# Performance work log

Hardware: AMD Instinct MI355X
Metric: run time of the kernel (lower is better)

## Reference

```python
import jax, jax.numpy as jnp
import numpy as np

DIM = 384
HEADS = 6
HEAD_DIM = DIM // HEADS
HIDDEN = 4 * DIM
K_NEIGH = 8
EPS = 1e-5


def layer_norm(x, w, b):
    mu = jnp.mean(x, axis=-1, keepdims=True)
    var = jnp.mean(jnp.square(x - mu), axis=-1, keepdims=True)
    return (x - mu) * jax.lax.rsqrt(var + EPS) * w + b


def setup_inputs() -> dict:
    key = jax.random.key(0)
    ks = jax.random.split(key, 16)
    B, N, D = 8, 2048, DIM
    s = 0.02
    inp = {
        "x": jax.random.normal(ks[0], (B, N, D), dtype=jnp.float32),
        "knn_index": jax.random.randint(ks[1], (B * K_NEIGH * N,), 0, B * N, dtype=jnp.int64),
        "norm1_w": jnp.ones((D,), jnp.float32),
        "norm1_b": jnp.zeros((D,), jnp.float32),
        "qkv_w": jax.random.normal(ks[2], (D, 3 * D), jnp.float32) * s,
        "proj_w": jax.random.normal(ks[3], (D, D), jnp.float32) * s,
        "proj_b": jnp.zeros((D,), jnp.float32),
        "knn_w": jax.random.normal(ks[4], (2 * D, D), jnp.float32) * s,
        "knn_b": jnp.zeros((D,), jnp.float32),
        "merge_w": jax.random.normal(ks[5], (2 * D, D), jnp.float32) * s,
        "merge_b": jnp.zeros((D,), jnp.float32),
        "norm2_w": jnp.ones((D,), jnp.float32),
        "norm2_b": jnp.zeros((D,), jnp.float32),
        "fc1_w": jax.random.normal(ks[6], (D, HIDDEN), jnp.float32) * s,
        "fc1_b": jnp.zeros((HIDDEN,), jnp.float32),
        "fc2_w": jax.random.normal(ks[7], (HIDDEN, D), jnp.float32) * s,
        "fc2_b": jnp.zeros((D,), jnp.float32),
    }
    return inp


def _forward(x, knn_index, norm1_w, norm1_b, qkv_w, proj_w, proj_b,
             knn_w, knn_b, merge_w, merge_b, norm2_w, norm2_b,
             fc1_w, fc1_b, fc2_w, fc2_b):
    B, N, D = x.shape
    norm_x = layer_norm(x, norm1_w, norm1_b)

    # --- multi-head self-attention (no qkv bias, no dropout) ---
    qkv = (norm_x @ qkv_w).reshape(B, N, 3, HEADS, HEAD_DIM)
    q, k, v = qkv[:, :, 0], qkv[:, :, 1], qkv[:, :, 2]  # [B,N,H,Dh]
    scale = HEAD_DIM ** -0.5
    attn = jnp.einsum("bnhd,bmhd->bhnm", q, k) * scale
    attn = jax.nn.softmax(attn, axis=-1)
    x_1 = jnp.einsum("bhnm,bmhd->bnhd", attn, v).reshape(B, N, D)
    x_1 = x_1 @ proj_w + proj_b

    # --- graph feature: gather k=8 neighbors, diff-concat ---
    feat = norm_x.reshape(B * N, D)[knn_index].reshape(B, K_NEIGH, N, D)
    xq = norm_x[:, None]  # [B,1,N,D]
    knn_f = jnp.concatenate([feat - xq, jnp.broadcast_to(xq, feat.shape)], axis=-1)
    knn_f = jax.nn.leaky_relu(knn_f @ knn_w + knn_b, negative_slope=0.2)
    knn_f = jnp.max(knn_f, axis=1)  # max-pool over neighbors -> [B,N,D]

    x_1 = jnp.concatenate([x_1, knn_f], axis=-1) @ merge_w + merge_b
    x = x + x_1

    # --- MLP block ---
    h = layer_norm(x, norm2_w, norm2_b)
    h = jax.nn.gelu(h @ fc1_w + fc1_b, approximate=False)
    x = x + (h @ fc2_w + fc2_b)
    return x


def reference(x, knn_index, norm1_w, norm1_b, qkv_w, proj_w, proj_b,
              knn_w, knn_b, merge_w, merge_b, norm2_w, norm2_b,
              fc1_w, fc1_b, fc2_w, fc2_b):
    return _forward(x, knn_index, norm1_w, norm1_b, qkv_w, proj_w, proj_b,
                    knn_w, knn_b, merge_w, merge_b, norm2_w, norm2_b,
                    fc1_w, fc1_b, fc2_w, fc2_b)
```

## Files before the change

kernel.cpp:

```cpp
#include <hip/hip_runtime.h>

typedef unsigned short u16;
typedef unsigned int u32;
typedef __attribute__((ext_vector_type(8))) short short8;
typedef __attribute__((ext_vector_type(4))) u16 u16x4;
typedef __attribute__((ext_vector_type(2))) u32 u32x2;
typedef __attribute__((ext_vector_type(4))) float f32x4;

__device__ __forceinline__ u16 f2bf(float f) {
  unsigned u = __float_as_uint(f);
  u += 0x7fffu + ((u >> 16) & 1u);
  return (u16)(u >> 16);
}
__device__ __forceinline__ float b2f(u16 v) { return __uint_as_float((u32)v << 16); }

#define GLD16(g, l)                                                        \
  __builtin_amdgcn_global_load_lds(                                        \
      (const __attribute__((address_space(1))) void*)(g),                  \
      (__attribute__((address_space(3))) void*)(l), 16, 0, 0)

struct TJobs {
  const float* in[7];
  unsigned long long outoff[7];
  int ld[7], row0[7], K[7], blkend[7];
};
__global__ void transpose_all_kernel(TJobs J, char* __restrict__ ws) {
  int bx = blockIdx.x;
  int ji = 0;
  while (bx >= J.blkend[ji]) ji++;
  int base = (ji == 0) ? 0 : J.blkend[ji - 1];
  int i = (bx - base) * 256 + threadIdx.x;
  int K = J.K[ji];
  int j = i / K, k = i - j * K;
  u16* out = (u16*)(ws + J.outoff[ji]);
  out[(size_t)j * K + k] = f2bf(J.in[ji][(size_t)(J.row0[ji] + k) * J.ld[ji] + j]);
}

__global__ void ln_kernel(const float* __restrict__ in, const float* __restrict__ w,
                          const float* __restrict__ b, u16* __restrict__ out) {
  int row = blockIdx.x, t = threadIdx.x;
  const float* r = in + (size_t)row * 384;
  float v[6];
  float s = 0.f;
#pragma unroll
  for (int i = 0; i < 6; i++) { v[i] = r[t + 64 * i]; s += v[i]; }
#pragma unroll
  for (int off = 32; off > 0; off >>= 1) s += __shfl_xor(s, off);
  float mu = s * (1.f / 384.f);
  float q = 0.f;
#pragma unroll
  for (int i = 0; i < 6; i++) { float d = v[i] - mu; q += d * d; }
#pragma unroll
  for (int off = 32; off > 0; off >>= 1) q += __shfl_xor(q, off);
  float rstd = rsqrtf(q * (1.f / 384.f) + 1e-5f);
#pragma unroll
  for (int i = 0; i < 6; i++) {
    int j = t + 64 * i;
    out[(size_t)row * 384 + j] = f2bf((v[i] - mu) * rstd * w[j] + b[j]);
  }
}

template <int MODE, int TN>
__global__ __launch_bounds__(256) void gemm_kernel(
    const u16* __restrict__ A, const u16* __restrict__ Bt,
    int M, int N, int K, int ldc,
    const float* __restrict__ bias, const float* __restrict__ res,
    void* __restrict__ out0, void* __restrict__ out1, void* __restrict__ out2,
    void* __restrict__ out3) {
  __shared__ u16 Als[2][128 * 32];
  __shared__ u16 Bls[2][TN * 32];
  const int NJ = TN / 32;
  const int MB = M >> 7;
  int mb = blockIdx.x % MB, nb = blockIdx.x / MB;
  int m0 = mb << 7, n0 = nb * TN;
  int tid = threadIdx.x;
  int lane = tid & 63, w = tid >> 6;
  int wm = (w >> 1) << 6, wn = (w & 1) * (TN / 2);
  int l15 = lane & 15, l16 = lane >> 4;
  const f32x4 fz = {0.f, 0.f, 0.f, 0.f};
  f32x4 acc[4][NJ];
#pragma unroll
  for (int i = 0; i < 4; i++)
#pragma unroll
    for (int j = 0; j < NJ; j++) acc[i][j] = fz;

  const int strow = lane >> 2, stch = (lane & 3) * 8;
  const u16* Ag = A + (size_t)(m0 + w * 32 + strow) * K + stch;
  const u16* Bg = Bt + (size_t)(n0 + w * (TN / 4) + strow) * K + stch;
  u16* Al0 = &Als[0][(w * 32) * 32];
  u16* Al1 = &Als[1][(w * 32) * 32];
  u16* Bl0 = &Bls[0][(w * (TN / 4)) * 32];
  u16* Bl1 = &Bls[1][(w * (TN / 4)) * 32];

  for (int k0 = 0; k0 < K; k0 += 64) {
    __syncthreads();
    GLD16(Ag + k0, Al0);
    GLD16(Ag + k0 + (size_t)16 * K, Al0 + 16 * 32);
    GLD16(Ag + k0 + 32, Al1);
    GLD16(Ag + k0 + 32 + (size_t)16 * K, Al1 + 16 * 32);
    GLD16(Bg + k0, Bl0);
    GLD16(Bg + k0 + 32, Bl1);
    if (TN == 128) {
      GLD16(Bg + k0 + (size_t)16 * K, Bl0 + 16 * 32);
      GLD16(Bg + k0 + 32 + (size_t)16 * K, Bl1 + 16 * 32);
    }
    asm volatile("s_waitcnt vmcnt(0)" ::: "memory");
    __syncthreads();
#pragma unroll
    for (int kk = 0; kk < 2; kk++) {
      short8 af[4], bfr[NJ];
#pragma unroll
      for (int i = 0; i < 4; i++)
        af[i] = *(const short8*)&Als[kk][(wm + i * 16 + l15) * 32 + l16 * 8];
#pragma unroll
      for (int j = 0; j < NJ; j++)
        bfr[j] = *(const short8*)&Bls[kk][(wn + j * 16 + l15) * 32 + l16 * 8];
      __builtin_amdgcn_s_setprio(1);
#pragma unroll
      for (int i = 0; i < 4; i++)
#pragma unroll
        for (int j = 0; j < NJ; j++)
          acc[i][j] = __builtin_amdgcn_mfma_f32_16x16x32_bf16(af[i], bfr[j], acc[i][j], 0, 0, 0);
      __builtin_amdgcn_s_setprio(0);
    }
  }

#pragma unroll
  for (int i = 0; i < 4; i++)
#pragma unroll
    for (int j = 0; j < NJ; j++)
#pragma unroll
      for (int r = 0; r < 4; r++) {
        int row = m0 + wm + i * 16 + l16 * 4 + r;
        int col = n0 + wn + j * 16 + l15;
        float v = acc[i][j][r];
        if (MODE == 1) {
          ((u16*)out0)[(size_t)row * ldc + col] = f2bf(v + bias[col]);
        } else if (MODE == 2) {
          if (col < 384) {
            ((u16*)out0)[(size_t)row * 384 + col] = f2bf(v * 0.18033688011112042f);
          } else if (col < 768) {
            ((u16*)out1)[(size_t)row * 384 + col - 384] = f2bf(v);
          } else if (col < 1152) {
            int df = col - 768, hh = df >> 6, dd = df & 63;
            ((u16*)out2)[(((size_t)(row >> 11) * 6 + hh) * 64 + dd) * 2048 + (row & 2047)] = f2bf(v);
          } else {
            ((u16*)out3)[(size_t)row * 768 + (col - 1152)] = f2bf(v);
          }
        } else if (MODE == 3) {
          ((float*)out0)[(size_t)row * ldc + col] = v + bias[col] + res[(size_t)row * ldc + col];
        } else if (MODE == 4) {
          float u = v + bias[col];
          float t = u * (0.79788456f + 0.03567741f * u * u);
          float g = u / (1.f + exp2f(-2.88539008f * t));
          ((u16*)out0)[(size_t)row * ldc + col] = f2bf(g);
        }
      }
}

#define ASTR 80
__global__ __launch_bounds__(256) void attn_kernel(const u16* __restrict__ qb,
                                                   const u16* __restrict__ kb,
                                                   const u16* __restrict__ vtb,
                                                   u16* __restrict__ ab) {
  __shared__ u16 Kls[64 * ASTR];
  __shared__ u16 Vls[64 * ASTR];
  __shared__ u16 Pls[64 * ASTR];
  int bx = blockIdx.x;
  int q0 = (bx & 31) << 6;
  int h = (bx >> 5) % 6;
  int b = bx / 192;
  int tid = threadIdx.x, lane = tid & 63, w = tid >> 6;
  int l15 = lane & 15, l16 = lane >> 4;

  const size_t qbase = (size_t)(b * 2048 + q0) * 384 + h * 64;
  {
    int idx0 = tid, idx1 = 256 + tid;
    *(short8*)&Kls[(idx0 >> 3) * ASTR + (idx0 & 7) * 8] =
        *(const short8*)&qb[qbase + (size_t)(idx0 >> 3) * 384 + (idx0 & 7) * 8];
    *(short8*)&Kls[(idx1 >> 3) * ASTR + (idx1 & 7) * 8] =
        *(const short8*)&qb[qbase + (size_t)(idx1 >> 3) * 384 + (idx1 & 7) * 8];
  }
  __syncthreads();
  short8 aq0 = *(const short8*)&Kls[(w * 16 + l15) * ASTR + l16 * 8];
  short8 aq1 = *(const short8*)&Kls[(w * 16 + l15) * ASTR + 32 + l16 * 8];

  const f32x4 fz = {0.f, 0.f, 0.f, 0.f};
  f32x4 ot[4];
  f32x4 osum;
#pragma unroll
  for (int di = 0; di < 4; di++) ot[di] = fz;
  osum = fz;
  short8 ones8;
#pragma unroll
  for (int i = 0; i < 8; i++) ones8[i] = (short)0x3F80;

  const size_t kbase = (size_t)b * 2048 * 384 + h * 64;
  const size_t vbase = ((size_t)b * 6 + h) * 64 * 2048;
  const int srow = tid >> 3, sch = (tid & 7) * 8;

  short8 kr0 = *(const short8*)&kb[kbase + (size_t)srow * 384 + sch];
  short8 kr1 = *(const short8*)&kb[kbase + (size_t)(srow + 32) * 384 + sch];
  short8 vr0 = *(const short8*)&vtb[vbase + (size_t)srow * 2048 + sch];
  short8 vr1 = *(const short8*)&vtb[vbase + (size_t)(srow + 32) * 2048 + sch];

  for (int t = 0; t < 32; t++) {
    __syncthreads();
    *(short8*)&Kls[srow * ASTR + sch] = kr0;
    *(short8*)&Kls[(srow + 32) * ASTR + sch] = kr1;
    *(short8*)&Vls[srow * ASTR + sch] = vr0;
    *(short8*)&Vls[(srow + 32) * ASTR + sch] = vr1;
    if (t + 1 < 32) {
      int j0n = (t + 1) << 6;
      kr0 = *(const short8*)&kb[kbase + (size_t)(j0n + srow) * 384 + sch];
      kr1 = *(const short8*)&kb[kbase + (size_t)(j0n + srow + 32) * 384 + sch];
      vr0 = *(const short8*)&vtb[vbase + (size_t)srow * 2048 + j0n + sch];
      vr1 = *(const short8*)&vtb[vbase + (size_t)(srow + 32) * 2048 + j0n + sch];
    }
    __syncthreads();

    f32x4 s[4];
    __builtin_amdgcn_s_setprio(1);
#pragma unroll
    for (int nj = 0; nj < 4; nj++) {
      short8 kf0 = *(const short8*)&Kls[(nj * 16 + l15) * ASTR + l16 * 8];
      short8 kf1 = *(const short8*)&Kls[(nj * 16 + l15) * ASTR + 32 + l16 * 8];
      s[nj] = __builtin_amdgcn_mfma_f32_16x16x32_bf16(kf0, aq0, fz, 0, 0, 0);
      s[nj] = __builtin_amdgcn_mfma_f32_16x16x32_bf16(kf1, aq1, s[nj], 0, 0, 0);
    }
    __builtin_amdgcn_s_setprio(0);

#pragma unroll
    for (int nj = 0; nj < 4; nj++) {
      float p0 = exp2f(s[nj][0]);
      float p1 = exp2f(s[nj][1]);
      float p2 = exp2f(s[nj][2]);
      float p3 = exp2f(s[nj][3]);
      u32 lo = (__float_as_uint(p1) & 0xffff0000u) | (__float_as_uint(p0) >> 16);
      u32 hi = (__float_as_uint(p3) & 0xffff0000u) | (__float_as_uint(p2) >> 16);
      u32x2 pr = {lo, hi};
      *(u32x2*)&Pls[(w * 16 + l15) * ASTR + nj * 16 + l16 * 4] = pr;
    }

    __builtin_amdgcn_s_setprio(1);
#pragma unroll
    for (int ks = 0; ks < 2; ks++) {
      short8 pb = *(const short8*)&Pls[(w * 16 + l15) * ASTR + ks * 32 + l16 * 8];
      osum = __builtin_amdgcn_mfma_f32_16x16x32_bf16(ones8, pb, osum, 0, 0, 0);
#pragma unroll
      for (int di = 0; di < 4; di++) {
        short8 vf = *(const short8*)&Vls[(di * 16 + l15) * ASTR + ks * 32 + l16 * 8];
        ot[di] = __builtin_amdgcn_mfma_f32_16x16x32_bf16(vf, pb, ot[di], 0, 0, 0);
      }
    }
    __builtin_amdgcn_s_setprio(0);
  }

  float inv = 1.f / osum[0];
  int token = b * 2048 + q0 + w * 16 + l15;
#pragma unroll
  for (int di = 0; di < 4; di++) {
    u16x4 pk4 = {f2bf(ot[di][0] * inv), f2bf(ot[di][1] * inv),
                 f2bf(ot[di][2] * inv), f2bf(ot[di][3] * inv)};
    *(u16x4*)&ab[(size_t)token * 384 + h * 64 + di * 16 + l16 * 4] = pk4;
  }
}

__global__ void knn_kernel(const u16* __restrict__ GH, const int* __restrict__ kidx,
                           const float* __restrict__ kbias, u16* __restrict__ cat) {
  int f = blockIdx.x * 256 + threadIdx.x;
  if (f >= 16384 * 96) return;
  int token = f / 96, j4 = f - token * 96;
  int b = token >> 11, n = token & 2047;
  int j = j4 * 4;
  u16x4 gs = *(const u16x4*)&GH[(size_t)token * 768 + j];
  u16x4 hs = *(const u16x4*)&GH[(size_t)token * 768 + 384 + j];
  float4 kb4 = *(const float4*)&kbias[j];
  float dx = b2f(hs[0]) - b2f(gs[0]) + kb4.x;
  float dy = b2f(hs[1]) - b2f(gs[1]) + kb4.y;
  float dz = b2f(hs[2]) - b2f(gs[2]) + kb4.z;
  float dw = b2f(hs[3]) - b2f(gs[3]) + kb4.w;
  float mx = -1e30f, my = -1e30f, mz = -1e30f, mw = -1e30f;
#pragma unroll
  for (int k = 0; k < 8; k++) {
    int t = kidx[(b * 8 + k) * 2048 + n];
    u16x4 g = *(const u16x4*)&GH[(size_t)t * 768 + j];
    mx = fmaxf(mx, b2f(g[0]) + dx);
    my = fmaxf(my, b2f(g[1]) + dy);
    mz = fmaxf(mz, b2f(g[2]) + dz);
    mw = fmaxf(mw, b2f(g[3]) + dw);
  }
  mx = mx > 0.f ? mx : 0.2f * mx;
  my = my > 0.f ? my : 0.2f * my;
  mz = mz > 0.f ? mz : 0.2f * mz;
  mw = mw > 0.f ? mw : 0.2f * mw;
  u16x4 pk = {f2bf(mx), f2bf(my), f2bf(mz), f2bf(mw)};
  *(u16x4*)&cat[(size_t)token * 768 + 384 + j] = pk;
}

extern "C" void kernel_launch(void* const* d_in, const int* in_sizes, int n_in,
                              void* d_out, int out_size, void* d_ws, size_t ws_size,
                              hipStream_t stream) {
  const float* x       = (const float*)d_in[0];
  const int*   kidx    = (const int*)d_in[1];
  const float* n1w     = (const float*)d_in[2];
  const float* n1b     = (const float*)d_in[3];
  const float* qkv_w   = (const float*)d_in[4];
  const float* proj_w  = (const float*)d_in[5];
  const float* proj_b  = (const float*)d_in[6];
  const float* knn_w   = (const float*)d_in[7];
  const float* knn_b   = (const float*)d_in[8];
  const float* merge_w = (const float*)d_in[9];
  const float* merge_b = (const float*)d_in[10];
  const float* n2w     = (const float*)d_in[11];
  const float* n2b     = (const float*)d_in[12];
  const float* fc1_w   = (const float*)d_in[13];
  const float* fc1_b   = (const float*)d_in[14];
  const float* fc2_w   = (const float*)d_in[15];
  const float* fc2_b   = (const float*)d_in[16];
  float* out = (float*)d_out;
  char* ws = (char*)d_ws;

  u16* wbig   = (u16*)(ws + 0);
  u16* wproj  = (u16*)(ws + 1474560);
  u16* wmerge = (u16*)(ws + 1769472);
  u16* wfc1   = (u16*)(ws + 2359296);
  u16* wfc2   = (u16*)(ws + 3538944);
  u16* nx     = (u16*)(ws + 4718592);
  u16* qbf    = (u16*)(ws + 17301504);
  u16* kbf    = (u16*)(ws + 29884416);
  u16* vtb    = (u16*)(ws + 42467328);
  u16* GH     = (u16*)(ws + 55050240);
  float* xmid = (float*)(ws + 105381888);
  u16* cat = kbf;
  u16* n2  = qbf;
  u16* abf = nx;
  u16* hbf = GH;

  TJobs J;
  J.in[0] = qkv_w;   J.outoff[0] = 0;       J.ld[0] = 1152; J.row0[0] = 0;   J.K[0] = 384;  J.blkend[0] = 1728;
  J.in[1] = knn_w;   J.outoff[1] = 884736;  J.ld[1] = 384;  J.row0[1] = 0;   J.K[1] = 384;  J.blkend[1] = 2304;
  J.in[2] = knn_w;   J.outoff[2] = 1179648; J.ld[2] = 384;  J.row0[2] = 384; J.K[2] = 384;  J.blkend[2] = 2880;
  J.in[3] = proj_w;  J.outoff[3] = 1474560; J.ld[3] = 384;  J.row0[3] = 0;   J.K[3] = 384;  J.blkend[3] = 3456;
  J.in[4] = merge_w; J.outoff[4] = 1769472; J.ld[4] = 384;  J.row0[4] = 0;   J.K[4] = 768;  J.blkend[4] = 4608;
  J.in[5] = fc1_w;   J.outoff[5] = 2359296; J.ld[5] = 1536; J.row0[5] = 0;   J.K[5] = 384;  J.blkend[5] = 6912;
  J.in[6] = fc2_w;   J.outoff[6] = 3538944; J.ld[6] = 384;  J.row0[6] = 0;   J.K[6] = 1536; J.blkend[6] = 9216;
  transpose_all_kernel<<<9216, 256, 0, stream>>>(J, ws);

  ln_kernel<<<16384, 64, 0, stream>>>(x, n1w, n1b, nx);
  gemm_kernel<2, 128><<<128 * 15, 256, 0, stream>>>(nx, wbig, 16384, 1920, 384, 0, nullptr, nullptr, qbf, kbf, vtb, GH);
  attn_kernel<<<1536, 256, 0, stream>>>(qbf, kbf, vtb, abf);
  knn_kernel<<<6144, 256, 0, stream>>>(GH, kidx, knn_b, cat);
  gemm_kernel<1, 64><<<128 * 6, 256, 0, stream>>>(abf, wproj, 16384, 384, 384, 768, proj_b, nullptr, cat, nullptr, nullptr, nullptr);
  gemm_kernel<3, 64><<<128 * 6, 256, 0, stream>>>(cat, wmerge, 16384, 384, 768, 384, merge_b, x, xmid, nullptr, nullptr, nullptr);
  ln_kernel<<<16384, 64, 0, stream>>>(xmid, n2w, n2b, n2);
  gemm_kernel<4, 128><<<128 * 12, 256, 0, stream>>>(n2, wfc1, 16384, 1536, 384, 1536, fc1_b, nullptr, hbf, nullptr, nullptr, nullptr);
  gemm_kernel<3, 64><<<128 * 6, 256, 0, stream>>>(hbf, wfc2, 16384, 384, 1536, 384, fc2_b, xmid, out, nullptr, nullptr, nullptr);
}
```

Baseline: 302.0 us.

## Double attention query tile to 128 rows with 512-thread blocks sharing K/V tiles

The attention kernel now processes 128 query rows per block using 8 waves instead of 64 rows with 4 waves, halving the grid. Each K/V tile staged in LDS is reused by twice as many waves, which halves global K/V traffic per query and the per-thread staging loads. Q is staged through the enlarged P buffer. The trade-off is fewer blocks, more LDS per block, and larger barrier groups, which may hurt occupancy or latency hiding. Correctness depends on the unseen softmax/P section handling 8 waves.

```diff
diff --git a/kernel.cpp b/kernel.cpp
--- a/kernel.cpp
+++ b/kernel.cpp
@@ -159,31 +159,31 @@
 }
 
 #define ASTR 80
-__global__ __launch_bounds__(256) void attn_kernel(const u16* __restrict__ qb,
+__global__ __launch_bounds__(512) void attn_kernel(const u16* __restrict__ qb,
                                                    const u16* __restrict__ kb,
                                                    const u16* __restrict__ vtb,
                                                    u16* __restrict__ ab) {
   __shared__ u16 Kls[64 * ASTR];
   __shared__ u16 Vls[64 * ASTR];
-  __shared__ u16 Pls[64 * ASTR];
+  __shared__ u16 Pls[128 * ASTR];
   int bx = blockIdx.x;
-  int q0 = (bx & 31) << 6;
-  int h = (bx >> 5) % 6;
-  int b = bx / 192;
+  int q0 = (bx & 15) << 7;
+  int h = (bx >> 4) % 6;
+  int b = bx / 96;
   int tid = threadIdx.x, lane = tid & 63, w = tid >> 6;
   int l15 = lane & 15, l16 = lane >> 4;
 
   const size_t qbase = (size_t)(b * 2048 + q0) * 384 + h * 64;
   {
-    int idx0 = tid, idx1 = 256 + tid;
-    *(short8*)&Kls[(idx0 >> 3) * ASTR + (idx0 & 7) * 8] =
-        *(const short8*)&qb[qbase + (size_t)(idx0 >> 3) * 384 + (idx0 & 7) * 8];
-    *(short8*)&Kls[(idx1 >> 3) * ASTR + (idx1 & 7) * 8] =
-        *(const short8*)&qb[qbase + (size_t)(idx1 >> 3) * 384 + (idx1 & 7) * 8];
+    int i0 = tid, i1 = 512 + tid;
+    *(short8*)&Pls[(i0 >> 3) * ASTR + (i0 & 7) * 8] =
+        *(const short8*)&qb[qbase + (size_t)(i0 >> 3) * 384 + (i0 & 7) * 8];
+    *(short8*)&Pls[(i1 >> 3) * ASTR + (i1 & 7) * 8] =
+        *(const short8*)&qb[qbase + (size_t)(i1 >> 3) * 384 + (i1 & 7) * 8];
   }
   __syncthreads();
-  short8 aq0 = *(const short8*)&Kls[(w * 16 + l15) * ASTR + l16 * 8];
-  short8 aq1 = *(const short8*)&Kls[(w * 16 + l15) * ASTR + 32 + l16 * 8];
+  short8 aq0 = *(const short8*)&Pls[(w * 16 + l15) * ASTR + l16 * 8];
+  short8 aq1 = *(const short8*)&Pls[(w * 16 + l15) * ASTR + 32 + l16 * 8];
 
   const f32x4 fz = {0.f, 0.f, 0.f, 0.f};
   f32x4 ot[4];
@@ -199,23 +199,17 @@
   const size_t vbase = ((size_t)b * 6 + h) * 64 * 2048;
   const int srow = tid >> 3, sch = (tid & 7) * 8;
 
-  short8 kr0 = *(const short8*)&kb[kbase + (size_t)srow * 384 + sch];
-  short8 kr1 = *(const short8*)&kb[kbase + (size_t)(srow + 32) * 384 + sch];
-  short8 vr0 = *(const short8*)&vtb[vbase + (size_t)srow * 2048 + sch];
-  short8 vr1 = *(const short8*)&vtb[vbase + (size_t)(srow + 32) * 2048 + sch];
+  short8 kr = *(const short8*)&kb[kbase + (size_t)srow * 384 + sch];
+  short8 vr = *(const short8*)&vtb[vbase + (size_t)srow * 2048 + sch];
 
   for (int t = 0; t < 32; t++) {
     __syncthreads();
-    *(short8*)&Kls[srow * ASTR + sch] = kr0;
-    *(short8*)&Kls[(srow + 32) * ASTR + sch] = kr1;
-    *(short8*)&Vls[srow * ASTR + sch] = vr0;
-    *(short8*)&Vls[(srow + 32) * ASTR + sch] = vr1;
+    *(short8*)&Kls[srow * ASTR + sch] = kr;
+    *(short8*)&Vls[srow * ASTR + sch] = vr;
     if (t + 1 < 32) {
       int j0n = (t + 1) << 6;
-      kr0 = *(const short8*)&kb[kbase + (size_t)(j0n + srow) * 384 + sch];
-      kr1 = *(const short8*)&kb[kbase + (size_t)(j0n + srow + 32) * 384 + sch];
-      vr0 = *(const short8*)&vtb[vbase + (size_t)srow * 2048 + j0n + sch];
-      vr1 = *(const short8*)&vtb[vbase + (size_t)(srow + 32) * 2048 + j0n + sch];
+      kr = *(const short8*)&kb[kbase + (size_t)(j0n + srow) * 384 + sch];
+      vr = *(const short8*)&vtb[vbase + (size_t)srow * 2048 + j0n + sch];
     }
     __syncthreads();
 
@@ -349,7 +343,7 @@
 
   ln_kernel<<<16384, 64, 0, stream>>>(x, n1w, n1b, nx);
   gemm_kernel<2, 128><<<128 * 15, 256, 0, stream>>>(nx, wbig, 16384, 1920, 384, 0, nullptr, nullptr, qbf, kbf, vtb, GH);
-  attn_kernel<<<1536, 256, 0, stream>>>(qbf, kbf, vtb, abf);
+  attn_kernel<<<768, 512, 0, stream>>>(qbf, kbf, vtb, abf);
   knn_kernel<<<6144, 256, 0, stream>>>(GH, kidx, knn_b, cat);
   gemm_kernel<1, 64><<<128 * 6, 256, 0, stream>>>(abf, wproj, 16384, 384, 384, 768, proj_b, nullptr, cat, nullptr, nullptr, nullptr);
   gemm_kernel<3, 64><<<128 * 6, 256, 0, stream>>>(cat, wmerge, 16384, 384, 768, 384, merge_b, x, xmid, nullptr, nullptr, nullptr);
```

Result: faster. 285.4 us (-5.5%).
